# Kernel tuning notes

Hardware: AMD Instinct MI355X
Metric: run time of the kernel (lower is better)

Reference implementation:

```python
import jax, jax.numpy as jnp
import numpy as np

# Model config (matches init_kwargs)
L_F, DELTA_F, L_S, DELTA_S = 1, 1, 32, 16
HIDDEN = 32       # SSM state dim H
GRU_H = 64        # slow-branch GRU hidden
N_GRU = 4
B, T = 4, 32768


def setup_inputs() -> dict:
    key = jax.random.key(0)
    ks = jax.random.split(key, 13)
    def nrm(k, shape, s=0.05):
        return jax.random.normal(k, shape, dtype=jnp.float32) * s
    return {
        "x": jax.random.normal(ks[0], (B, T), dtype=jnp.float32),
        # SlowBranch params
        "fc_in_w": nrm(ks[1], (GRU_H, 1), 0.3),
        "fc_in_b": nrm(ks[2], (GRU_H,)),
        "gru_wih": nrm(ks[3], (N_GRU, 3 * GRU_H, GRU_H), 0.1),
        "gru_whh": nrm(ks[4], (N_GRU, 3 * GRU_H, GRU_H), 0.1),
        "gru_bih": nrm(ks[5], (N_GRU, 3 * GRU_H)),
        "gru_bhh": nrm(ks[6], (N_GRU, 3 * GRU_H)),
        "out_fc_w": nrm(ks[7], (2 * HIDDEN, GRU_H), 0.1),
        "out_fc_b": nrm(ks[8], (2 * HIDDEN,)),
        # Fast branch params (F_IN: 1->H, F_OUT: H->1)
        "fin_w": nrm(ks[9], (HIDDEN, 1), 0.3),
        "fin_b": nrm(ks[10], (HIDDEN,)),
        "fout_w": nrm(ks[11], (1, HIDDEN), 0.1),
        "fout_b": nrm(ks[12], (1,)),
    }


def _gru_layer(xs, Wih, Whh, bih, bhh):
    """Torch-convention GRU layer. xs: (N, L, H_in) -> (N, L, H)."""
    H = Whh.shape[1]
    # Precompute input-side gate pre-activations: (N, L, 3H)
    xp = jnp.einsum('nlh,gh->nlg', xs, Wih) + bih
    def step(h, xt):
        gh = h @ Whh.T + bhh                       # (N, 3H)
        ir, iz, inew = jnp.split(xt, 3, axis=-1)
        hr, hz, hnew = jnp.split(gh, 3, axis=-1)
        r = jax.nn.sigmoid(ir + hr)
        z = jax.nn.sigmoid(iz + hz)
        n = jnp.tanh(inew + r * hnew)
        h = (1.0 - z) * n + z * h
        return h, h
    h0 = jnp.zeros((xs.shape[0], H), xs.dtype)
    _, ys = jax.lax.scan(step, h0, jnp.swapaxes(xp, 0, 1))  # (L, N, H)
    return jnp.swapaxes(ys, 0, 1)


def reference(x, fc_in_w, fc_in_b, gru_wih, gru_whh, gru_bih, gru_bhh,
              out_fc_w, out_fc_b, fin_w, fin_b, fout_w, fout_b):
    Bsz, Tlen = x.shape
    num_slow = (Tlen - L_S) // DELTA_S + 1

    frame_idx = jnp.arange(num_slow)[:, None] * DELTA_S + jnp.arange(L_S)[None, :]
    x_s = x[:, frame_idx].reshape(Bsz * num_slow, L_S, 1)      # (N, L_s, 1)
    h = jax.nn.relu(x_s * fc_in_w[:, 0] + fc_in_b)             # (N, L_s, GRU_H)
    for l in range(gru_wih.shape[0]):
        h = _gru_layer(h, gru_wih[l], gru_whh[l], gru_bih[l], gru_bhh[l])
    eps = h[:, -1, :] @ out_fc_w.T + out_fc_b                  # (N, 2H)
    eps = eps.reshape(Bsz, num_slow, 2 * HIDDEN)
    A_slow = jax.nn.sigmoid(eps[..., :HIDDEN])                 # (B, S, H)
    g_slow = eps[..., HIDDEN:]                                 # (B, S, H)

    # ---- Fast branch: per-sample diagonal linear SSM scan ----
    delta = DELTA_S // DELTA_F
    idx = jnp.clip(jnp.arange(Tlen) // delta - 1, 0, num_slow - 1)  # (T,)
    A_t = A_slow[:, idx, :]                                    # (B, T, H)
    u_t = (x[..., None] * fin_w[:, 0] + fin_b) * g_slow[:, idx, :]  # (B, T, H)

    def step(hc, inp):
        A, u = inp
        hn = A * hc + u
        return hn, hn
    h0 = jnp.zeros((Bsz, HIDDEN), x.dtype)
    _, h_all = jax.lax.scan(step, h0,
                            (jnp.swapaxes(A_t, 0, 1), jnp.swapaxes(u_t, 0, 1)))
    # h_all: (T, B, H); F_OUT applied to every state
    return jnp.einsum('tbh,h->bt', h_all, fout_w[0]) + fout_b[0]   # (B, T)
```

## Files before the change

kernel.cpp:

```cpp
#include <hip/hip_runtime.h>
#include <hip/hip_bf16.h>

typedef __bf16 bf16x8 __attribute__((ext_vector_type(8)));
typedef short short8 __attribute__((ext_vector_type(8)));
typedef float f32x4 __attribute__((ext_vector_type(4)));
typedef unsigned short ushort_t;

#define T_LEN 32768
#define B_SZ 4
#define NSLOW 2047
#define NSEQ (B_SZ * NSLOW)
#define GH 64
#define G3 192
#define NL 4
#define HID 32
#define L2E 1.44269504088896341f

#define OFF_X    0
#define OFF_FCW  131072
#define OFF_FCB  131136
#define OFF_WIH  131200
#define OFF_WHH  180352
#define OFF_BIH  229504
#define OFF_BHH  230272
#define OFF_OFW  231040
#define OFF_OFB  235136
#define OFF_FINW 235200
#define OFF_FINB 235232
#define OFF_FOW  235264
#define OFF_FOB  235296
#define CONV_TOTAL 235297
#define CONV_PAD_BYTES 470656

static __device__ __forceinline__ float bf2f(ushort_t u) {
    union { unsigned u; float f; } c; c.u = ((unsigned)u) << 16; return c.f;
}
static __device__ __forceinline__ ushort_t f2bf(float f) {
    union { float f; unsigned u; } c; c.f = f;
    unsigned r = (c.u + 0x7FFFu + ((c.u >> 16) & 1u)) >> 16;
    return (ushort_t)r;
}
static __device__ __forceinline__ f32x4 mfma16(short8 a, short8 b, f32x4 c) {
    return __builtin_amdgcn_mfma_f32_16x16x32_bf16(
        __builtin_bit_cast(bf16x8, a), __builtin_bit_cast(bf16x8, b), c, 0, 0, 0);
}
static __device__ __forceinline__ int xoff(int t, int kb, int seq) {
    return ((((t << 3) + kb) << 4) + (seq ^ ((kb & 3) << 2))) << 3;
}
static __device__ __forceinline__ short8 load_frag_scaled(const ushort_t* p, float s) {
    uint4 r = *(const uint4*)p;
    unsigned aa[4] = {r.x, r.y, r.z, r.w};
    short8 o;
#pragma unroll
    for (int i = 0; i < 4; ++i) {
        o[2 * i]     = (short)f2bf(bf2f((ushort_t)(aa[i] & 0xffffu)) * s);
        o[2 * i + 1] = (short)f2bf(bf2f((ushort_t)(aa[i] >> 16)) * s);
    }
    return o;
}

__global__ __launch_bounds__(64) void detect_kernel(const ushort_t* __restrict__ x,
                                                    int* __restrict__ flag)
{
    int lane = threadIdx.x;
    int cnt = 0;
#pragma unroll
    for (int i = 0; i < 4; ++i) {
        ushort_t u = x[lane * 4 + i];
        int e = (u >> 7) & 0xFF;
        if (e >= 80 && e <= 141) cnt++;
    }
#pragma unroll
    for (int d = 1; d < 64; d <<= 1) cnt += __shfl_xor(cnt, d, 64);
    if (lane == 0) *flag = (cnt >= 224) ? 1 : 0;
}

struct Ptrs13 { const void* p[13]; };

__global__ __launch_bounds__(256) void convert_kernel(Ptrs13 ptrs,
                                                      const int* __restrict__ flag,
                                                      ushort_t* __restrict__ dst)
{
    const int offs[14] = {OFF_X, OFF_FCW, OFF_FCB, OFF_WIH, OFF_WHH, OFF_BIH,
                          OFF_BHH, OFF_OFW, OFF_OFB, OFF_FINW, OFF_FINB,
                          OFF_FOW, OFF_FOB, CONV_TOTAL};
    const bool isbf = (*flag != 0);
    for (int idx = blockIdx.x * 256 + threadIdx.x; idx < CONV_TOTAL;
         idx += gridDim.x * 256) {
        int s = 0;
#pragma unroll
        for (int j = 1; j < 13; ++j) if (idx >= offs[j]) s = j;
        int k = idx - offs[s];
        ushort_t v = isbf ? ((const ushort_t*)ptrs.p[s])[k]
                          : f2bf(((const float*)ptrs.p[s])[k]);
        dst[idx] = v;
    }
}

__global__ __launch_bounds__(256) void gru_kernel(
    const ushort_t* __restrict__ x, const ushort_t* __restrict__ fcw,
    const ushort_t* __restrict__ fcb, const ushort_t* __restrict__ wih,
    const ushort_t* __restrict__ whh, const ushort_t* __restrict__ bih,
    const ushort_t* __restrict__ bhh, const ushort_t* __restrict__ ofw,
    const ushort_t* __restrict__ ofb, float* __restrict__ Aslow,
    float* __restrict__ gslow)
{
    __shared__ short8 Xs8[4096];
    short* Xs = (short*)Xs8;
    const int tid = threadIdx.x;
    const int w = tid >> 6, lane = tid & 63;
    const int q = lane >> 4, m = lane & 15;
    const int jb = w * 16;
    const int n0 = blockIdx.x * 16;

#pragma unroll 1
    for (int ii = 0; ii < 16; ++ii) {
        int cid = ii * 256 + tid;
        int seq = cid & 15, kb = (cid >> 4) & 7, t = cid >> 7;
        int n = n0 + seq; if (n > NSEQ - 1) n = NSEQ - 1;
        int b = n / NSLOW, s = n - b * NSLOW;
        float xv = bf2f(x[b * T_LEN + s * 16 + t]);
        short8 v;
#pragma unroll
        for (int i = 0; i < 8; ++i) {
            int g = kb * 8 + i;
            float h = fmaf(xv, bf2f(fcw[g]), bf2f(fcb[g]));
            h = h > 0.f ? h : 0.f;
            v[i] = (short)f2bf(h);
        }
        Xs8[xoff(t, kb, seq) >> 3] = v;
    }

    const int kb_w = 2 * w + (m >> 3);
    const int i7 = m & 7;
    const int wsz = (kb_w & 3) << 2;
    const int colR = jb + m;

    float hc[4];
#pragma unroll 1
    for (int l = 0; l < NL; ++l) {
        const ushort_t* wl = wih + l * G3 * GH;
        const ushort_t* ul = whh + l * G3 * GH;
        const int kofs = q * 8;
        short8 wR0 = load_frag_scaled(wl + (0 * 64 + colR) * 64 + kofs, -L2E);
        short8 wR1 = load_frag_scaled(wl + (0 * 64 + colR) * 64 + 32 + kofs, -L2E);
        short8 wZ0 = load_frag_scaled(wl + (1 * 64 + colR) * 64 + kofs, -L2E);
        short8 wZ1 = load_frag_scaled(wl + (1 * 64 + colR) * 64 + 32 + kofs, -L2E);
        short8 wN0 = load_frag_scaled(wl + (2 * 64 + colR) * 64 + kofs, 2.f * L2E);
        short8 wN1 = load_frag_scaled(wl + (2 * 64 + colR) * 64 + 32 + kofs, 2.f * L2E);
        short8 uR0 = load_frag_scaled(ul + (0 * 64 + colR) * 64 + kofs, -L2E);
        short8 uR1 = load_frag_scaled(ul + (0 * 64 + colR) * 64 + 32 + kofs, -L2E);
        short8 uZ0 = load_frag_scaled(ul + (1 * 64 + colR) * 64 + kofs, -L2E);
        short8 uZ1 = load_frag_scaled(ul + (1 * 64 + colR) * 64 + 32 + kofs, -L2E);
        short8 uN0 = load_frag_scaled(ul + (2 * 64 + colR) * 64 + kofs, 2.f * L2E);
        short8 uN1 = load_frag_scaled(ul + (2 * 64 + colR) * 64 + 32 + kofs, 2.f * L2E);

        float bR  = -L2E * (bf2f(bih[l * G3 + colR]) + bf2f(bhh[l * G3 + colR]));
        float bZ  = -L2E * (bf2f(bih[l * G3 + 64 + colR]) + bf2f(bhh[l * G3 + 64 + colR]));
        float bNX = 2.f * L2E * bf2f(bih[l * G3 + 128 + colR]);
        float bNH = 2.f * L2E * bf2f(bhh[l * G3 + 128 + colR]);

        hc[0] = hc[1] = hc[2] = hc[3] = 0.f;

#pragma unroll 1
        for (int t = 0; t < 32; ++t) {
            __syncthreads();
            short8 ax0 = Xs8[xoff(t, q, m) >> 3];
            short8 ax1 = Xs8[xoff(t, 4 + q, m) >> 3];
            short8 ah0 = ax0, ah1 = ax1;
            if (t > 0) {
                ah0 = Xs8[xoff(t - 1, q, m) >> 3];
                ah1 = Xs8[xoff(t - 1, 4 + q, m) >> 3];
            }
            __syncthreads();
            f32x4 aR  = {bR, bR, bR, bR};
            f32x4 aZ  = {bZ, bZ, bZ, bZ};
            f32x4 aNX = {bNX, bNX, bNX, bNX};
            f32x4 aNH = {bNH, bNH, bNH, bNH};
            aR  = mfma16(ax0, wR0, aR);  aR  = mfma16(ax1, wR1, aR);
            aZ  = mfma16(ax0, wZ0, aZ);  aZ  = mfma16(ax1, wZ1, aZ);
            aNX = mfma16(ax0, wN0, aNX); aNX = mfma16(ax1, wN1, aNX);
            if (t > 0) {
                aR  = mfma16(ah0, uR0, aR);  aR  = mfma16(ah1, uR1, aR);
                aZ  = mfma16(ah0, uZ0, aZ);  aZ  = mfma16(ah1, uZ1, aZ);
                aNH = mfma16(ah0, uN0, aNH); aNH = mfma16(ah1, uN1, aNH);
            }
#pragma unroll
            for (int i = 0; i < 4; ++i) {
                float r = __builtin_amdgcn_rcpf(1.f + __builtin_amdgcn_exp2f(aR[i]));
                float z = __builtin_amdgcn_rcpf(1.f + __builtin_amdgcn_exp2f(aZ[i]));
                float yp = fmaf(r, aNH[i], aNX[i]);
                float nn = fmaf(-2.f,
                    __builtin_amdgcn_rcpf(1.f + __builtin_amdgcn_exp2f(yp)), 1.f);
                hc[i] = fmaf(z, hc[i] - nn, nn);
                int seq = 4 * q + i;
                Xs[((((t << 3) + kb_w) << 4) + (seq ^ wsz)) * 8 + i7] =
                    (short)f2bf(hc[i]);
            }
        }
    }

    __syncthreads();
    short8 aL0 = Xs8[xoff(31, q, m) >> 3];
    short8 aL1 = Xs8[xoff(31, 4 + q, m) >> 3];
    const int colO = jb + m;
    float sc = (w < 2) ? -L2E : 1.f;
    short8 o0 = load_frag_scaled(ofw + colO * 64 + q * 8, sc);
    short8 o1 = load_frag_scaled(ofw + colO * 64 + 32 + q * 8, sc);
    float be = bf2f(ofb[colO]) * sc;
    f32x4 aE = {be, be, be, be};
    aE = mfma16(aL0, o0, aE);
    aE = mfma16(aL1, o1, aE);
#pragma unroll
    for (int i = 0; i < 4; ++i) {
        int n = n0 + 4 * q + i;
        if (w < 2)
            Aslow[n * HID + colO] =
                __builtin_amdgcn_rcpf(1.f + __builtin_amdgcn_exp2f(aE[i]));
        else
            gslow[n * HID + (colO - 32)] = aE[i];
    }
}

__global__ __launch_bounds__(256) void pass1_kernel(
    const ushort_t* __restrict__ x, const float* __restrict__ Aslow,
    const float* __restrict__ gslow, const ushort_t* __restrict__ finw,
    const ushort_t* __restrict__ finb, float* __restrict__ P,
    float* __restrict__ S)
{
    int gt = blockIdx.x * 256 + threadIdx.x;
    int h = gt & 31, c = (gt >> 5) & 127, b = gt >> 12;
    float fw = bf2f(finw[h]), fb = bf2f(finb[h]);
    float Pv = 1.f, Sv = 0.f;
    int t0 = c * 256;
#pragma unroll 1
    for (int seg = 0; seg < 16; ++seg) {
        int sidx = (t0 >> 4) + seg - 1;
        if (sidx < 0) sidx = 0;
        if (sidx > NSLOW - 1) sidx = NSLOW - 1;
        float A = Aslow[(b * NSLOW + sidx) * HID + h];
        float g = gslow[(b * NSLOW + sidx) * HID + h];
        float fwg = fw * g, fbg = fb * g;
        const uint4* px = (const uint4*)(x + b * T_LEN + t0 + seg * 16);
        uint4 ra = px[0], rb = px[1];
        unsigned xa[8] = {ra.x, ra.y, ra.z, ra.w, rb.x, rb.y, rb.z, rb.w};
#pragma unroll
        for (int j = 0; j < 8; ++j) {
            float x0 = bf2f((ushort_t)(xa[j] & 0xffffu));
            float x1 = bf2f((ushort_t)(xa[j] >> 16));
            Sv = fmaf(A, Sv, fmaf(x0, fwg, fbg));
            Sv = fmaf(A, Sv, fmaf(x1, fwg, fbg));
        }
        float A2 = A * A, A4 = A2 * A2, A8 = A4 * A4;
        Pv *= A8 * A8;
    }
    P[(b * HID + h) * 128 + c] = Pv;
    S[(b * HID + h) * 128 + c] = Sv;
}

__global__ __launch_bounds__(128) void scan_kernel(
    const float* __restrict__ P, const float* __restrict__ S,
    float* __restrict__ Hpre)
{
    int tid = threadIdx.x;
    const float4* p4 = (const float4*)(P + tid * 128);
    const float4* s4 = (const float4*)(S + tid * 128);
    float* hp = Hpre + tid * 128;
    float hr = 0.f;
#pragma unroll 1
    for (int c = 0; c < 32; ++c) {
        float4 pv = p4[c], sv = s4[c];
        hp[4 * c + 0] = hr; hr = fmaf(pv.x, hr, sv.x);
        hp[4 * c + 1] = hr; hr = fmaf(pv.y, hr, sv.y);
        hp[4 * c + 2] = hr; hr = fmaf(pv.z, hr, sv.z);
        hp[4 * c + 3] = hr; hr = fmaf(pv.w, hr, sv.w);
    }
}

__global__ __launch_bounds__(256) void pass2_kernel(
    const ushort_t* __restrict__ x, const float* __restrict__ Aslow,
    const float* __restrict__ gslow, const float* __restrict__ Hpre,
    const ushort_t* __restrict__ finw, const ushort_t* __restrict__ finb,
    const ushort_t* __restrict__ fow, const ushort_t* __restrict__ fob,
    const int* __restrict__ flag, void* __restrict__ outv)
{
    int wv = blockIdx.x * 4 + (threadIdx.x >> 6);
    int lane = threadIdx.x & 63;
    int half = lane >> 5, h = lane & 31;
    int pair = wv * 2 + half;
    int b = pair >> 7, c = pair & 127;
    const bool isbf = (*flag != 0);
    ushort_t* outb = (ushort_t*)outv;
    float* outf = (float*)outv;
    float hv = Hpre[(b * HID + h) * 128 + c];
    float fw = bf2f(finw[h]), fb = bf2f(finb[h]);
    float wo = bf2f(fow[h]), ob = bf2f(fob[0]);
    int t0 = c * 256;
#pragma unroll 1
    for (int blk = 0; blk < 8; ++blk) {
        float ykeep = 0.f;
        float A = 0.f, fwg = 0.f, fbg = 0.f;
#pragma unroll
        for (int tt = 0; tt < 32; ++tt) {
            int t = t0 + blk * 32 + tt;
            if ((tt & 15) == 0) {
                int sidx = (t >> 4) - 1;
                if (sidx < 0) sidx = 0;
                A = Aslow[(b * NSLOW + sidx) * HID + h];
                float g = gslow[(b * NSLOW + sidx) * HID + h];
                fwg = fw * g; fbg = fb * g;
            }
            float xv = bf2f(x[b * T_LEN + t]);
            hv = fmaf(A, hv, fmaf(xv, fwg, fbg));
            float y = hv * wo;
            y += __shfl_xor(y, 1, 64);
            y += __shfl_xor(y, 2, 64);
            y += __shfl_xor(y, 4, 64);
            y += __shfl_xor(y, 8, 64);
            y += __shfl_xor(y, 16, 64);
            if (tt == h) ykeep = y + ob;
        }
        int oidx = b * T_LEN + t0 + blk * 32 + h;
        if (isbf) outb[oidx] = f2bf(ykeep);
        else      outf[oidx] = ykeep;
    }
}

extern "C" void kernel_launch(void* const* d_in, const int* in_sizes, int n_in,
                              void* d_out, int out_size, void* d_ws, size_t ws_size,
                              hipStream_t stream)
{
    ushort_t* cv = (ushort_t*)d_ws;
    const ushort_t* x    = cv + OFF_X;
    const ushort_t* fcw  = cv + OFF_FCW;
    const ushort_t* fcb  = cv + OFF_FCB;
    const ushort_t* wih  = cv + OFF_WIH;
    const ushort_t* whh  = cv + OFF_WHH;
    const ushort_t* bih  = cv + OFF_BIH;
    const ushort_t* bhh  = cv + OFF_BHH;
    const ushort_t* ofw  = cv + OFF_OFW;
    const ushort_t* ofb  = cv + OFF_OFB;
    const ushort_t* finw = cv + OFF_FINW;
    const ushort_t* finb = cv + OFF_FINB;
    const ushort_t* fow  = cv + OFF_FOW;
    const ushort_t* fob  = cv + OFF_FOB;

    float* Aslow = (float*)((char*)d_ws + CONV_PAD_BYTES);
    float* gslow = Aslow + 8192 * 32;
    float* P     = gslow + 8192 * 32;
    float* S     = P + 16384;
    float* Hpre  = S + 16384;
    int*   flag  = (int*)(Hpre + 16384);

    Ptrs13 ptrs;
    for (int i = 0; i < 13; ++i) ptrs.p[i] = d_in[i];

    detect_kernel<<<dim3(1), dim3(64), 0, stream>>>((const ushort_t*)d_in[0], flag);
    convert_kernel<<<dim3(920), dim3(256), 0, stream>>>(ptrs, flag, cv);
    gru_kernel<<<dim3(512), dim3(256), 0, stream>>>(
        x, fcw, fcb, wih, whh, bih, bhh, ofw, ofb, Aslow, gslow);
    pass1_kernel<<<dim3(64), dim3(256), 0, stream>>>(
        x, Aslow, gslow, finw, finb, P, S);
    scan_kernel<<<dim3(1), dim3(128), 0, stream>>>(P, S, Hpre);
    pass2_kernel<<<dim3(64), dim3(256), 0, stream>>>(
        x, Aslow, gslow, Hpre, finw, finb, fow, fob, flag, d_out);
}
```

Before: 213.8 us.

## Transpose GRU MFMA operands, prefetch LDS inputs, halve scan chunk size

The GRU step swaps the MFMA operand order so each lane owns four consecutive hidden columns of one sequence. That allows a packed 8-byte bf16 store of the new state in place of four scalar LDS stores, and it changes the LDS swizzle to match. The loop drops one barrier per timestep and prefetches the next timestep's input fragments from LDS. The fast-branch chunk count doubles from 128 to 256 per batch, so pass1 and pass2 run twice as many blocks, at the cost of a longer serial scan_kernel.

```diff
diff --git a/kernel.cpp b/kernel.cpp
--- a/kernel.cpp
+++ b/kernel.cpp
@@ -14,6 +14,7 @@
 #define G3 192
 #define NL 4
 #define HID 32
+#define NCH 256
 #define L2E 1.44269504088896341f
 
 #define OFF_X    0
@@ -40,12 +41,19 @@
     unsigned r = (c.u + 0x7FFFu + ((c.u >> 16) & 1u)) >> 16;
     return (ushort_t)r;
 }
+static __device__ __forceinline__ unsigned pk2bf(float a, float b) {
+    float2 f; f.x = a; f.y = b;
+    __hip_bfloat162 h = __float22bfloat162_rn(f);
+    unsigned u;
+    __builtin_memcpy(&u, &h, 4);
+    return u;
+}
 static __device__ __forceinline__ f32x4 mfma16(short8 a, short8 b, f32x4 c) {
     return __builtin_amdgcn_mfma_f32_16x16x32_bf16(
         __builtin_bit_cast(bf16x8, a), __builtin_bit_cast(bf16x8, b), c, 0, 0, 0);
 }
 static __device__ __forceinline__ int xoff(int t, int kb, int seq) {
-    return ((((t << 3) + kb) << 4) + (seq ^ ((kb & 3) << 2))) << 3;
+    return ((((t << 3) + kb) << 4) + (seq ^ (kb & 7))) << 3;
 }
 static __device__ __forceinline__ short8 load_frag_scaled(const ushort_t* p, float s) {
     uint4 r = *(const uint4*)p;
@@ -131,59 +139,73 @@
         Xs8[xoff(t, kb, seq) >> 3] = v;
     }
 
-    const int kb_w = 2 * w + (m >> 3);
-    const int i7 = m & 7;
-    const int wsz = (kb_w & 3) << 2;
-    const int colR = jb + m;
+    const int col0 = jb + 4 * q;
+    const int kbw = (col0 >> 3);
+    const int wsub = (col0 & 7);
+    const int kofs = q * 8;
+    const int wbase0 = ((kbw << 4) + (m ^ (kbw & 7))) * 8 + wsub;
 
     float hc[4];
 #pragma unroll 1
     for (int l = 0; l < NL; ++l) {
         const ushort_t* wl = wih + l * G3 * GH;
         const ushort_t* ul = whh + l * G3 * GH;
-        const int kofs = q * 8;
-        short8 wR0 = load_frag_scaled(wl + (0 * 64 + colR) * 64 + kofs, -L2E);
-        short8 wR1 = load_frag_scaled(wl + (0 * 64 + colR) * 64 + 32 + kofs, -L2E);
-        short8 wZ0 = load_frag_scaled(wl + (1 * 64 + colR) * 64 + kofs, -L2E);
-        short8 wZ1 = load_frag_scaled(wl + (1 * 64 + colR) * 64 + 32 + kofs, -L2E);
-        short8 wN0 = load_frag_scaled(wl + (2 * 64 + colR) * 64 + kofs, 2.f * L2E);
-        short8 wN1 = load_frag_scaled(wl + (2 * 64 + colR) * 64 + 32 + kofs, 2.f * L2E);
-        short8 uR0 = load_frag_scaled(ul + (0 * 64 + colR) * 64 + kofs, -L2E);
-        short8 uR1 = load_frag_scaled(ul + (0 * 64 + colR) * 64 + 32 + kofs, -L2E);
-        short8 uZ0 = load_frag_scaled(ul + (1 * 64 + colR) * 64 + kofs, -L2E);
-        short8 uZ1 = load_frag_scaled(ul + (1 * 64 + colR) * 64 + 32 + kofs, -L2E);
-        short8 uN0 = load_frag_scaled(ul + (2 * 64 + colR) * 64 + kofs, 2.f * L2E);
-        short8 uN1 = load_frag_scaled(ul + (2 * 64 + colR) * 64 + 32 + kofs, 2.f * L2E);
-
-        float bR  = -L2E * (bf2f(bih[l * G3 + colR]) + bf2f(bhh[l * G3 + colR]));
-        float bZ  = -L2E * (bf2f(bih[l * G3 + 64 + colR]) + bf2f(bhh[l * G3 + 64 + colR]));
-        float bNX = 2.f * L2E * bf2f(bih[l * G3 + 128 + colR]);
-        float bNH = 2.f * L2E * bf2f(bhh[l * G3 + 128 + colR]);
+        short8 wR0 = load_frag_scaled(wl + (0 * 64 + jb + m) * 64 + kofs, -L2E);
+        short8 wR1 = load_frag_scaled(wl + (0 * 64 + jb + m) * 64 + 32 + kofs, -L2E);
+        short8 wZ0 = load_frag_scaled(wl + (1 * 64 + jb + m) * 64 + kofs, -L2E);
+        short8 wZ1 = load_frag_scaled(wl + (1 * 64 + jb + m) * 64 + 32 + kofs, -L2E);
+        short8 wN0 = load_frag_scaled(wl + (2 * 64 + jb + m) * 64 + kofs, 2.f * L2E);
+        short8 wN1 = load_frag_scaled(wl + (2 * 64 + jb + m) * 64 + 32 + kofs, 2.f * L2E);
+        short8 uR0 = load_frag_scaled(ul + (0 * 64 + jb + m) * 64 + kofs, -L2E);
+        short8 uR1 = load_frag_scaled(ul + (0 * 64 + jb + m) * 64 + 32 + kofs, -L2E);
+        short8 uZ0 = load_frag_scaled(ul + (1 * 64 + jb + m) * 64 + kofs, -L2E);
+        short8 uZ1 = load_frag_scaled(ul + (1 * 64 + jb + m) * 64 + 32 + kofs, -L2E);
+        short8 uN0 = load_frag_scaled(ul + (2 * 64 + jb + m) * 64 + kofs, 2.f * L2E);
+        short8 uN1 = load_frag_scaled(ul + (2 * 64 + jb + m) * 64 + 32 + kofs, 2.f * L2E);
+
+        float bR[4], bZ[4], bNX[4], bNH[4];
+#pragma unroll
+        for (int i = 0; i < 4; ++i) {
+            int c = col0 + i;
+            bR[i]  = -L2E * (bf2f(bih[l * G3 + c]) + bf2f(bhh[l * G3 + c]));
+            bZ[i]  = -L2E * (bf2f(bih[l * G3 + 64 + c]) + bf2f(bhh[l * G3 + 64 + c]));
+            bNX[i] = 2.f * L2E * bf2f(bih[l * G3 + 128 + c]);
+            bNH[i] = 2.f * L2E * bf2f(bhh[l * G3 + 128 + c]);
+        }
 
         hc[0] = hc[1] = hc[2] = hc[3] = 0.f;
+
+        __syncthreads();
+        int iA = xoff(0, q, m) >> 3;
+        int iB = xoff(0, 4 + q, m) >> 3;
+        short8 bx0 = Xs8[iA];
+        short8 bx1 = Xs8[iB];
+        int wb = wbase0;
 
 #pragma unroll 1
         for (int t = 0; t < 32; ++t) {
             __syncthreads();
-            short8 ax0 = Xs8[xoff(t, q, m) >> 3];
-            short8 ax1 = Xs8[xoff(t, 4 + q, m) >> 3];
-            short8 ah0 = ax0, ah1 = ax1;
+            short8 bh0 = bx0, bh1 = bx1;
             if (t > 0) {
-                ah0 = Xs8[xoff(t - 1, q, m) >> 3];
-                ah1 = Xs8[xoff(t - 1, 4 + q, m) >> 3];
-            }
-            __syncthreads();
-            f32x4 aR  = {bR, bR, bR, bR};
-            f32x4 aZ  = {bZ, bZ, bZ, bZ};
-            f32x4 aNX = {bNX, bNX, bNX, bNX};
-            f32x4 aNH = {bNH, bNH, bNH, bNH};
-            aR  = mfma16(ax0, wR0, aR);  aR  = mfma16(ax1, wR1, aR);
-            aZ  = mfma16(ax0, wZ0, aZ);  aZ  = mfma16(ax1, wZ1, aZ);
-            aNX = mfma16(ax0, wN0, aNX); aNX = mfma16(ax1, wN1, aNX);
+                bh0 = Xs8[iA - 128];
+                bh1 = Xs8[iB - 128];
+            }
+            short8 nx0 = bx0, nx1 = bx1;
+            if (t < 31) {
+                nx0 = Xs8[iA + 128];
+                nx1 = Xs8[iB + 128];
+            }
+            f32x4 aR  = {bR[0], bR[1], bR[2], bR[3]};
+            f32x4 aZ  = {bZ[0], bZ[1], bZ[2], bZ[3]};
+            f32x4 aNX = {bNX[0], bNX[1], bNX[2], bNX[3]};
+            f32x4 aNH = {bNH[0], bNH[1], bNH[2], bNH[3]};
+            aR  = mfma16(wR0, bx0, aR);  aR  = mfma16(wR1, bx1, aR);
+            aZ  = mfma16(wZ0, bx0, aZ);  aZ  = mfma16(wZ1, bx1, aZ);
+            aNX = mfma16(wN0, bx0, aNX); aNX = mfma16(wN1, bx1, aNX);
             if (t > 0) {
-                aR  = mfma16(ah0, uR0, aR);  aR  = mfma16(ah1, uR1, aR);
-                aZ  = mfma16(ah0, uZ0, aZ);  aZ  = mfma16(ah1, uZ1, aZ);
-                aNH = mfma16(ah0, uN0, aNH); aNH = mfma16(ah1, uN1, aNH);
+                aR  = mfma16(uR0, bh0, aR);  aR  = mfma16(uR1, bh1, aR);
+                aZ  = mfma16(uZ0, bh0, aZ);  aZ  = mfma16(uZ1, bh1, aZ);
+                aNH = mfma16(uN0, bh0, aNH); aNH = mfma16(uN1, bh1, aNH);
             }
 #pragma unroll
             for (int i = 0; i < 4; ++i) {
@@ -193,32 +215,34 @@
                 float nn = fmaf(-2.f,
                     __builtin_amdgcn_rcpf(1.f + __builtin_amdgcn_exp2f(yp)), 1.f);
                 hc[i] = fmaf(z, hc[i] - nn, nn);
-                int seq = 4 * q + i;
-                Xs[((((t << 3) + kb_w) << 4) + (seq ^ wsz)) * 8 + i7] =
-                    (short)f2bf(hc[i]);
-            }
+            }
+            unsigned lo = pk2bf(hc[0], hc[1]);
+            unsigned hi = pk2bf(hc[2], hc[3]);
+            *(uint2*)(Xs + wb) = make_uint2(lo, hi);
+            bx0 = nx0; bx1 = nx1;
+            iA += 128; iB += 128; wb += 1024;
         }
     }
 
     __syncthreads();
     short8 aL0 = Xs8[xoff(31, q, m) >> 3];
     short8 aL1 = Xs8[xoff(31, 4 + q, m) >> 3];
-    const int colO = jb + m;
     float sc = (w < 2) ? -L2E : 1.f;
-    short8 o0 = load_frag_scaled(ofw + colO * 64 + q * 8, sc);
-    short8 o1 = load_frag_scaled(ofw + colO * 64 + 32 + q * 8, sc);
-    float be = bf2f(ofb[colO]) * sc;
-    f32x4 aE = {be, be, be, be};
-    aE = mfma16(aL0, o0, aE);
-    aE = mfma16(aL1, o1, aE);
-#pragma unroll
-    for (int i = 0; i < 4; ++i) {
-        int n = n0 + 4 * q + i;
-        if (w < 2)
-            Aslow[n * HID + colO] =
-                __builtin_amdgcn_rcpf(1.f + __builtin_amdgcn_exp2f(aE[i]));
-        else
-            gslow[n * HID + (colO - 32)] = aE[i];
+    short8 o0 = load_frag_scaled(ofw + (jb + m) * 64 + kofs, sc);
+    short8 o1 = load_frag_scaled(ofw + (jb + m) * 64 + 32 + kofs, sc);
+    f32x4 aE = {bf2f(ofb[col0]) * sc, bf2f(ofb[col0 + 1]) * sc,
+                bf2f(ofb[col0 + 2]) * sc, bf2f(ofb[col0 + 3]) * sc};
+    aE = mfma16(o0, aL0, aE);
+    aE = mfma16(o1, aL1, aE);
+    int n = n0 + m;
+    if (w < 2) {
+        f32x4 v;
+#pragma unroll
+        for (int i = 0; i < 4; ++i)
+            v[i] = __builtin_amdgcn_rcpf(1.f + __builtin_amdgcn_exp2f(aE[i]));
+        *(f32x4*)(Aslow + n * HID + col0) = v;
+    } else {
+        *(f32x4*)(gslow + n * HID + (col0 - 32)) = aE;
     }
 }
 
@@ -229,12 +253,12 @@
     float* __restrict__ S)
 {
     int gt = blockIdx.x * 256 + threadIdx.x;
-    int h = gt & 31, c = (gt >> 5) & 127, b = gt >> 12;
+    int h = gt & 31, c = (gt >> 5) & 255, b = gt >> 13;
     float fw = bf2f(finw[h]), fb = bf2f(finb[h]);
     float Pv = 1.f, Sv = 0.f;
-    int t0 = c * 256;
-#pragma unroll 1
-    for (int seg = 0; seg < 16; ++seg) {
+    int t0 = c * 128;
+#pragma unroll 1
+    for (int seg = 0; seg < 8; ++seg) {
         int sidx = (t0 >> 4) + seg - 1;
         if (sidx < 0) sidx = 0;
         if (sidx > NSLOW - 1) sidx = NSLOW - 1;
@@ -254,8 +278,8 @@
         float A2 = A * A, A4 = A2 * A2, A8 = A4 * A4;
         Pv *= A8 * A8;
     }
-    P[(b * HID + h) * 128 + c] = Pv;
-    S[(b * HID + h) * 128 + c] = Sv;
+    P[(b * HID + h) * NCH + c] = Pv;
+    S[(b * HID + h) * NCH + c] = Sv;
 }
 
 __global__ __launch_bounds__(128) void scan_kernel(
@@ -263,12 +287,12 @@
     float* __restrict__ Hpre)
 {
     int tid = threadIdx.x;
-    const float4* p4 = (const float4*)(P + tid * 128);
-    const float4* s4 = (const float4*)(S + tid * 128);
-    float* hp = Hpre + tid * 128;
+    const float4* p4 = (const float4*)(P + tid * NCH);
+    const float4* s4 = (const float4*)(S + tid * NCH);
+    float* hp = Hpre + tid * NCH;
     float hr = 0.f;
 #pragma unroll 1
-    for (int c = 0; c < 32; ++c) {
+    for (int c = 0; c < NCH / 4; ++c) {
         float4 pv = p4[c], sv = s4[c];
         hp[4 * c + 0] = hr; hr = fmaf(pv.x, hr, sv.x);
         hp[4 * c + 1] = hr; hr = fmaf(pv.y, hr, sv.y);
@@ -288,16 +312,16 @@
     int lane = threadIdx.x & 63;
     int half = lane >> 5, h = lane & 31;
     int pair = wv * 2 + half;
-    int b = pair >> 7, c = pair & 127;
+    int b = pair >> 8, c = pair & 255;
     const bool isbf = (*flag != 0);
     ushort_t* outb = (ushort_t*)outv;
     float* outf = (float*)outv;
-    float hv = Hpre[(b * HID + h) * 128 + c];
+    float hv = Hpre[(b * HID + h) * NCH + c];
     float fw = bf2f(finw[h]), fb = bf2f(finb[h]);
     float wo = bf2f(fow[h]), ob = bf2f(fob[0]);
-    int t0 = c * 256;
-#pragma unroll 1
-    for (int blk = 0; blk < 8; ++blk) {
+    int t0 = c * 128;
+#pragma unroll 1
+    for (int blk = 0; blk < 4; ++blk) {
         float ykeep = 0.f;
         float A = 0.f, fwg = 0.f, fbg = 0.f;
 #pragma unroll
@@ -348,9 +372,9 @@
     float* Aslow = (float*)((char*)d_ws + CONV_PAD_BYTES);
     float* gslow = Aslow + 8192 * 32;
     float* P     = gslow + 8192 * 32;
-    float* S     = P + 16384;
-    float* Hpre  = S + 16384;
-    int*   flag  = (int*)(Hpre + 16384);
+    float* S     = P + 4 * 32 * NCH;
+    float* Hpre  = S + 4 * 32 * NCH;
+    int*   flag  = (int*)(Hpre + 4 * 32 * NCH);
 
     Ptrs13 ptrs;
     for (int i = 0; i < 13; ++i) ptrs.p[i] = d_in[i];
@@ -359,9 +383,9 @@
     convert_kernel<<<dim3(920), dim3(256), 0, stream>>>(ptrs, flag, cv);
     gru_kernel<<<dim3(512), dim3(256), 0, stream>>>(
         x, fcw, fcb, wih, whh, bih, bhh, ofw, ofb, Aslow, gslow);
-    pass1_kernel<<<dim3(64), dim3(256), 0, stream>>>(
+    pass1_kernel<<<dim3(128), dim3(256), 0, stream>>>(
         x, Aslow, gslow, finw, finb, P, S);
     scan_kernel<<<dim3(1), dim3(128), 0, stream>>>(P, S, Hpre);
-    pass2_kernel<<<dim3(64), dim3(256), 0, stream>>>(
+    pass2_kernel<<<dim3(128), dim3(256), 0, stream>>>(
         x, Aslow, gslow, Hpre, finw, finb, fow, fob, flag, d_out);
 }
```

After: 211.8 us. About the same (-0.9%).
